# Performance work log

Measured on AMD Instinct MI355X. Metric: run time of the kernel, lower is better.

## Reference

```python
import jax, jax.numpy as jnp
import numpy as np

BIG = 1e30  # finite stand-in for +inf to keep grads clean


def _chamfer_loss(bin_center, ground_truth):
    # bin_center: [B, n_bins, 1] 1-D 'point cloud' of bin centers
    # ground_truth: [B, 1, H, W] depth map
    B = bin_center.shape[0]
    c = bin_center[..., 0]                      # [B, nb]
    p = ground_truth.reshape(B, -1)             # [B, V] flattened depth points
    mask = p >= 0.001                           # valid (non-near-zero) depths
    n = jnp.sum(mask, axis=1)                   # [B] valid count per sample
    Lmax = jnp.max(n)                           # pad_sequence pads every sample to L_max
    npad = (Lmax - n).astype(c.dtype)           # number of zero pad-points per sample

    # pairwise squared distances between bin centers and depth points
    D = (c[:, :, None] - p[:, None, :]) ** 2    # [B, nb, V]

    # direction 1: gt points -> nearest bin center (sum over points)
    dmin_p = jnp.min(D, axis=1)                 # [B, V]
    sumA = jnp.sum(jnp.where(mask, dmin_p, 0.0), axis=1)
    # each zero pad-point contributes min_j c_j^2
    c2 = c ** 2                                 # [B, nb]
    sumA = sumA + npad * jnp.min(c2, axis=1)

    # direction 2: bin centers -> nearest gt point (incl. zero pad-points if any)
    Dm = jnp.where(mask[:, None, :], D, jnp.asarray(BIG, D.dtype))
    min_valid = jnp.min(Dm, axis=2)             # [B, nb] min over valid points
    has_pad = (npad > 0)[:, None]
    min_b = jnp.where(has_pad, jnp.minimum(min_valid, c2), min_valid)
    sumB = jnp.sum(min_b, axis=1)               # [B]

    # chamferdist: point_reduction=sum, batch_reduction=mean, bidirectional
    return jnp.mean(sumA + sumB)


def setup_inputs() -> dict:
    key = jax.random.key(0)
    k1, k2 = jax.random.split(key)
    bin_center = jax.random.uniform(k1, (4, 256, 1), dtype=jnp.float32)
    ground_truth = jax.random.uniform(k2, (4, 1, 352, 448), dtype=jnp.float32)
    return {"bin_center": bin_center, "ground_truth": ground_truth}


def reference(bin_center, ground_truth):
    return _chamfer_loss(bin_center, ground_truth)
```

## Files before the change

### kernel.cpp

```cpp
#include <hip/hip_runtime.h>

#define NB   256
#define TPB  256
#define NI   (NB + 1)
#define G    128
#define MINF 1e30f
#define CAPD 1e15f

__global__ __launch_bounds__(TPB) void k_fused(
    const float* __restrict__ bc, const float* __restrict__ gt,
    int B, int V, int CH,
    unsigned* __restrict__ gbin,
    unsigned* __restrict__ counter,
    unsigned* __restrict__ ssort,
    unsigned* __restrict__ sumP,
    unsigned* __restrict__ cntP,
    float* __restrict__ out)
{
    const int b   = blockIdx.x / G;
    const int blk = blockIdx.x % G;
    const int tid = threadIdx.x;

    __shared__ float    c[NB];
    __shared__ unsigned imn[NI], imx[NI];
    __shared__ float    pm[NB], sm[NB];
    __shared__ float r4[4]; __shared__ int i4[4]; __shared__ float q4[4];
    __shared__ float ssa[8]; __shared__ int sn[8];
    __shared__ unsigned s_old;

    c[tid] = bc[b * NB + tid];
    for (int t = tid; t < NI; t += TPB) { imn[t] = 0xFFFFFFFFu; imx[t] = 0u; }
    __syncthreads();

    for (int k = 2; k <= NB; k <<= 1)
        for (int j = k >> 1; j > 0; j >>= 1) {
            const int ixj = tid ^ j;
            if (ixj > tid) {
                const float a = c[tid], bv = c[ixj];
                if ((a > bv) == ((tid & k) == 0)) { c[tid] = bv; c[ixj] = a; }
            }
            __syncthreads();
        }

    if (blk == 0) atomicExch(&ssort[b * NB + tid], __float_as_uint(c[tid]));

    const int start = blk * CH;
    const int cn = min(CH, V - start);
    const float* __restrict__ gp = gt + (size_t)b * V + start;
    float sum = 0.f; int cnt = 0;
    for (int i = tid; i < cn; i += TPB) {
        const float q = gp[i];
        if (q >= 0.001f) {
            int idx = 0;
            #pragma unroll
            for (int st = 128; st >= 1; st >>= 1)
                idx += (c[idx + st - 1] <= q) ? st : 0;
            idx += (c[idx] <= q) ? 1 : 0;
            const float dlo = (idx > 0)  ? (q - c[idx - 1]) : MINF;
            const float dhi = (idx < NB) ? (c[idx] - q)     : MINF;
            const float d = fminf(dlo, dhi);
            sum += d * d; ++cnt;
            atomicMin(&imn[idx], __float_as_uint(q));
            atomicMax(&imx[idx], __float_as_uint(q));
        }
    }
    __syncthreads();

    pm[tid] = (imx[tid]     == 0u)          ? -MINF : __uint_as_float(imx[tid]);
    sm[tid] = (imn[tid + 1] == 0xFFFFFFFFu) ?  MINF : __uint_as_float(imn[tid + 1]);
    __syncthreads();
    for (int off = 1; off < NB; off <<= 1) {
        const float vp = pm[tid], vs = sm[tid];
        const float op = (tid >= off)     ? pm[tid - off] : -MINF;
        const float os = (tid + off < NB) ? sm[tid + off] :  MINF;
        __syncthreads();
        pm[tid] = fmaxf(vp, op);
        sm[tid] = fminf(vs, os);
        __syncthreads();
    }
    {
        const float cj = c[tid];
        const float d  = fminf(fminf(cj - pm[tid], sm[tid] - cj), CAPD);
        atomicMin(&gbin[b * NB + tid], __float_as_uint(d * d));
    }

    for (int off = 32; off; off >>= 1) {
        sum += __shfl_down(sum, off);
        cnt += __shfl_down(cnt, off);
    }
    if ((tid & 63) == 0) { r4[tid >> 6] = sum; i4[tid >> 6] = cnt; }
    __syncthreads();
    if (tid == 0) {
        atomicExch(&sumP[blockIdx.x], __float_as_uint(r4[0] + r4[1] + r4[2] + r4[3]));
        atomicExch(&cntP[blockIdx.x], (unsigned)(i4[0] + i4[1] + i4[2] + i4[3]));
    }

    __syncthreads();
    if (tid == 0) s_old = atomicAdd(counter, 1u);
    __syncthreads();
    if (s_old != (unsigned)(gridDim.x - 2)) return;
    __threadfence();

    for (int bb = 0; bb < B; ++bb) {
        float s = 0.f; int cc = 0;
        for (int k = tid; k < G; k += TPB) {
            s  += __uint_as_float(sumP[bb * G + k]);
            cc += (int)cntP[bb * G + k];
        }
        for (int off = 32; off; off >>= 1) { s += __shfl_down(s, off); cc += __shfl_down(cc, off); }
        if ((tid & 63) == 0) { r4[tid >> 6] = s; i4[tid >> 6] = cc; }
        __syncthreads();
        if (tid == 0) { ssa[bb] = r4[0]+r4[1]+r4[2]+r4[3]; sn[bb] = i4[0]+i4[1]+i4[2]+i4[3]; }
        __syncthreads();
    }
    int Lmax = 0;
    for (int bb = 0; bb < B; ++bb) Lmax = max(Lmax, sn[bb]);

    float total = 0.f;
    for (int bb = 0; bb < B; ++bb) {
        const int   npad = Lmax - sn[bb];
        const float cj = __uint_as_float(ssort[bb * NB + tid]);
        const float c2 = cj * cj;
        float bm = __uint_as_float(gbin[bb * NB + tid]);
        if (npad > 0) bm = fminf(bm, c2);
        float s = bm, mc = c2;
        for (int off = 32; off; off >>= 1) {
            s  += __shfl_down(s, off);
            mc  = fminf(mc, __shfl_down(mc, off));
        }
        if ((tid & 63) == 0) { r4[tid >> 6] = s; q4[tid >> 6] = mc; }
        __syncthreads();
        if (tid == 0)
            total += ssa[bb]
                   + (float)npad * fminf(fminf(q4[0], q4[1]), fminf(q4[2], q4[3]))
                   + (r4[0] + r4[1] + r4[2] + r4[3]);
        __syncthreads();
    }
    if (tid == 0) out[0] = total / (float)B;
}

extern "C" void kernel_launch(void* const* d_in, const int* in_sizes, int n_in,
                              void* d_out, int out_size, void* d_ws, size_t ws_size,
                              hipStream_t stream) {
    const float* bc = (const float*)d_in[0];
    const float* gt = (const float*)d_in[1];
    const int B  = in_sizes[0] / NB;
    const int V  = in_sizes[1] / B;
    const int CH = (V + G - 1) / G;

    unsigned* gbin    = (unsigned*)d_ws;
    unsigned* counter = gbin + (size_t)B * NB;
    unsigned* ssort   = counter + 1;
    unsigned* sumP    = ssort + (size_t)B * NB;
    unsigned* cntP    = sumP + (size_t)B * G;

    hipMemsetAsync(gbin, 0xFF, ((size_t)B * NB + 1) * sizeof(unsigned), stream);

    k_fused<<<B * G, TPB, 0, stream>>>(bc, gt, B, V, CH,
                                       gbin, counter, ssort, sumP, cntP,
                                       (float*)d_out);
}
```

Before: 79.45 us.

## Hoist bin sort into a separate kernel and batch binary searches per thread

```diff
diff --git a/kernel.cpp b/kernel.cpp
--- a/kernel.cpp
+++ b/kernel.cpp
@@ -3,16 +3,38 @@
 #define NB   256
 #define TPB  256
 #define NI   (NB + 1)
-#define G    128
+#define G    256
+#define PPT  3
 #define MINF 1e30f
 #define CAPD 1e15f
 
-__global__ __launch_bounds__(TPB) void k_fused(
-    const float* __restrict__ bc, const float* __restrict__ gt,
+__global__ __launch_bounds__(NB) void k_sort(const float* __restrict__ bc,
+                                             float* __restrict__ sbins,
+                                             unsigned* __restrict__ gbin,
+                                             unsigned* __restrict__ counter) {
+    __shared__ float s[NB];
+    const int tid = threadIdx.x, b = blockIdx.x;
+    s[tid] = bc[b * NB + tid];
+    gbin[b * NB + tid] = 0xFFFFFFFFu;
+    if (b == 0 && tid == 0) counter[0] = 0u;
+    __syncthreads();
+    for (int k = 2; k <= NB; k <<= 1)
+        for (int j = k >> 1; j > 0; j >>= 1) {
+            const int ixj = tid ^ j;
+            if (ixj > tid) {
+                const float a = s[tid], bv = s[ixj];
+                if ((a > bv) == ((tid & k) == 0)) { s[tid] = bv; s[ixj] = a; }
+            }
+            __syncthreads();
+        }
+    sbins[b * NB + tid] = s[tid];
+}
+
+__global__ __launch_bounds__(TPB) void k_main(
+    const float* __restrict__ sbins, const float* __restrict__ gt,
     int B, int V, int CH,
     unsigned* __restrict__ gbin,
     unsigned* __restrict__ counter,
-    unsigned* __restrict__ ssort,
     unsigned* __restrict__ sumP,
     unsigned* __restrict__ cntP,
     float* __restrict__ out)
@@ -28,40 +50,46 @@
     __shared__ float ssa[8]; __shared__ int sn[8];
     __shared__ unsigned s_old;
 
-    c[tid] = bc[b * NB + tid];
+    c[tid] = sbins[b * NB + tid];
     for (int t = tid; t < NI; t += TPB) { imn[t] = 0xFFFFFFFFu; imx[t] = 0u; }
-    __syncthreads();
-
-    for (int k = 2; k <= NB; k <<= 1)
-        for (int j = k >> 1; j > 0; j >>= 1) {
-            const int ixj = tid ^ j;
-            if (ixj > tid) {
-                const float a = c[tid], bv = c[ixj];
-                if ((a > bv) == ((tid & k) == 0)) { c[tid] = bv; c[ixj] = a; }
-            }
-            __syncthreads();
-        }
-
-    if (blk == 0) atomicExch(&ssort[b * NB + tid], __float_as_uint(c[tid]));
 
     const int start = blk * CH;
     const int cn = min(CH, V - start);
     const float* __restrict__ gp = gt + (size_t)b * V + start;
+
+    float q[PPT]; bool ok[PPT]; int idx[PPT];
+    #pragma unroll
+    for (int k = 0; k < PPT; ++k) {
+        const int i = tid + k * TPB;
+        const float v = (i < cn) ? gp[i] : 0.f;
+        ok[k]  = (i < cn) && (v >= 0.001f);
+        q[k]   = ok[k] ? v : 0.5f;
+        idx[k] = 0;
+    }
+    __syncthreads();
+
+    #pragma unroll
+    for (int st = 128; st >= 8; st >>= 1) {
+        #pragma unroll
+        for (int k = 0; k < PPT; ++k)
+            idx[k] += (c[idx[k] + st - 1] <= q[k]) ? st : 0;
+    }
     float sum = 0.f; int cnt = 0;
-    for (int i = tid; i < cn; i += TPB) {
-        const float q = gp[i];
-        if (q >= 0.001f) {
-            int idx = 0;
-            #pragma unroll
-            for (int st = 128; st >= 1; st >>= 1)
-                idx += (c[idx + st - 1] <= q) ? st : 0;
-            idx += (c[idx] <= q) ? 1 : 0;
-            const float dlo = (idx > 0)  ? (q - c[idx - 1]) : MINF;
-            const float dhi = (idx < NB) ? (c[idx] - q)     : MINF;
-            const float d = fminf(dlo, dhi);
-            sum += d * d; ++cnt;
-            atomicMin(&imn[idx], __float_as_uint(q));
-            atomicMax(&imx[idx], __float_as_uint(q));
+    #pragma unroll
+    for (int k = 0; k < PPT; ++k) {
+        const float4 w0 = *(const float4*)&c[idx[k]];
+        const float4 w1 = *(const float4*)&c[idx[k] + 4];
+        const int c8 = (w0.x <= q[k]) + (w0.y <= q[k]) + (w0.z <= q[k]) + (w0.w <= q[k])
+                     + (w1.x <= q[k]) + (w1.y <= q[k]) + (w1.z <= q[k]) + (w1.w <= q[k]);
+        const int L = idx[k] + c8;
+        const float dlo = (L > 0)  ? (q[k] - c[L - 1]) : MINF;
+        const float dhi = (L < NB) ? (c[L] - q[k])     : MINF;
+        const float d = fminf(dlo, dhi);
+        sum += ok[k] ? d * d : 0.f;
+        cnt += ok[k] ? 1 : 0;
+        if (ok[k]) {
+            atomicMin(&imn[L], __float_as_uint(q[k]));
+            atomicMax(&imx[L], __float_as_uint(q[k]));
         }
     }
     __syncthreads();
@@ -98,7 +126,7 @@
     __syncthreads();
     if (tid == 0) s_old = atomicAdd(counter, 1u);
     __syncthreads();
-    if (s_old != (unsigned)(gridDim.x - 2)) return;
+    if (s_old != (unsigned)(gridDim.x - 1)) return;
     __threadfence();
 
     for (int bb = 0; bb < B; ++bb) {
@@ -119,7 +147,7 @@
     float total = 0.f;
     for (int bb = 0; bb < B; ++bb) {
         const int   npad = Lmax - sn[bb];
-        const float cj = __uint_as_float(ssort[bb * NB + tid]);
+        const float cj = sbins[bb * NB + tid];
         const float c2 = cj * cj;
         float bm = __uint_as_float(gbin[bb * NB + tid]);
         if (npad > 0) bm = fminf(bm, c2);
@@ -148,15 +176,13 @@
     const int V  = in_sizes[1] / B;
     const int CH = (V + G - 1) / G;
 
-    unsigned* gbin    = (unsigned*)d_ws;
-    unsigned* counter = gbin + (size_t)B * NB;
-    unsigned* ssort   = counter + 1;
-    unsigned* sumP    = ssort + (size_t)B * NB;
+    float*    sbins   = (float*)d_ws;
+    unsigned* gbin    = (unsigned*)(sbins + (size_t)B*NB);
+    unsigned* sumP    = gbin + (size_t)B * NB;
     unsigned* cntP    = sumP + (size_t)B * G;
+    unsigned* counter = cntP + (size_t)B * G;
 
-    hipMemsetAsync(gbin, 0xFF, ((size_t)B * NB + 1) * sizeof(unsigned), stream);
-
-    k_fused<<<B * G, TPB, 0, stream>>>(bc, gt, B, V, CH,
-                                       gbin, counter, ssort, sumP, cntP,
-                                       (float*)d_out);
+    k_sort<<<B, NB, 0, stream>>>(bc, sbins, gbin, counter);
+    k_main<<<B * G, TPB, 0, stream>>>(sbins, gt, B, V, CH,
+                                      gbin, counter, sumP, cntP, (float*)d_out);
 }
```

Measured after the change: 81.68 us. 1.03x slower.
